# Performance work log

Hardware: AMD Instinct MI355X
Metric: run time of the kernel (lower is better)

The kernel has to match this reference:

```python
import jax, jax.numpy as jnp
import numpy as np

STATE = 1024

def setup_inputs() -> dict:
    key = jax.random.key(0)
    k1, k2, k3, k4, k5 = jax.random.split(key, 5)
    B, IN, S = 4096, 1024, STATE
    stdv = 1.0 / np.sqrt(S)
    return {
        "input": jax.random.normal(k1, (B, IN), jnp.float32),
        "old_h": jax.random.normal(k2, (B, S), jnp.float32),
        "old_cell": jax.random.normal(k3, (B, S), jnp.float32),
        "weights": jax.random.uniform(k4, (4 * S, IN + S), jnp.float32, -stdv, stdv),
        "bias": jax.random.uniform(k5, (4 * S,), jnp.float32, -stdv, stdv),
    }

def reference(input, old_h, old_cell, weights, bias):
    # Fused gate GEMM: X = [input, old_h] -> [B, IN+S]; gates -> [B, 4S]
    X = jnp.concatenate([input, old_h], axis=1)
    gates = X @ weights.T + bias
    f, i, o, g = jnp.split(gates, 4, axis=1)
    f = jax.nn.sigmoid(f)
    i = jax.nn.sigmoid(i)
    o = jax.nn.sigmoid(o)
    g = jnp.tanh(g)
    new_cell = f * old_cell + i * g
    new_h = o * jnp.tanh(new_cell)
    return new_h, new_cell
```

## Files before the change

### kernel.cpp

```cpp
#include <hip/hip_runtime.h>
#include <stdint.h>

#define NB   4096
#define KD   2048
#define ND   4096
#define SD   1024

#define BM   256
#define BN   256
#define BK   64
#define NKT  (KD / BK)

using f32x4  = __attribute__((ext_vector_type(4))) float;
using bf16x8 = __attribute__((ext_vector_type(8))) short;

typedef const __attribute__((address_space(1))) uint32_t* gas_u32;
typedef __attribute__((address_space(3))) uint32_t* las_u32;

__device__ __forceinline__ unsigned short f2bf(float f) {
    union { float f; uint32_t u; } c; c.f = f;
    uint32_t u = c.u;
    uint32_t r = (u + 0x7fffu + ((u >> 16) & 1u)) >> 16;
    return (unsigned short)r;
}

__device__ __forceinline__ void async_load16(const void* gsrc, void* ldst) {
    __builtin_amdgcn_global_load_lds((gas_u32)gsrc, (las_u32)ldst, 16, 0, 0);
}

__device__ __forceinline__ float frcp(float x) { return __builtin_amdgcn_rcpf(x); }
__device__ __forceinline__ float sigm(float x) { return frcp(1.f + __expf(-x)); }
__device__ __forceinline__ float tanh_fast(float x) {
    return 1.f - 2.f * frcp(1.f + __expf(2.f * x));
}

__global__ void pack_kernel(const float* __restrict__ input,
                            const float* __restrict__ old_h,
                            const float* __restrict__ weights,
                            const float* __restrict__ bias,
                            unsigned short* __restrict__ Xb,
                            unsigned short* __restrict__ Wb,
                            float* __restrict__ biasR) {
    const int XCH = NB * (KD / 4);
    const int WCH = ND * (KD / 4);
    const int BCH = ND / 4;
    const int total = XCH + WCH + BCH;
    for (int c = blockIdx.x * blockDim.x + threadIdx.x; c < total;
         c += gridDim.x * blockDim.x) {
        if (c < XCH) {
            int b  = c >> 9;
            int k  = (c & 511) << 2;
            const float* src = (k < 1024) ? (input + (size_t)b * 1024 + k)
                                          : (old_h + (size_t)b * 1024 + (k - 1024));
            float4 v = *reinterpret_cast<const float4*>(src);
            ushort4 o;
            o.x = f2bf(v.x); o.y = f2bf(v.y); o.z = f2bf(v.z); o.w = f2bf(v.w);
            *reinterpret_cast<ushort4*>(Xb + (size_t)b * KD + k) = o;
        } else if (c < XCH + WCH) {
            int cc = c - XCH;
            int n  = cc >> 9;
            int k  = (cc & 511) << 2;
            int srow = ((n >> 4) & 3) * SD + ((n >> 6) * 16 + (n & 15));
            float4 v = *reinterpret_cast<const float4*>(weights + (size_t)srow * KD + k);
            ushort4 o;
            o.x = f2bf(v.x); o.y = f2bf(v.y); o.z = f2bf(v.z); o.w = f2bf(v.w);
            *reinterpret_cast<ushort4*>(Wb + (size_t)n * KD + k) = o;
        } else {
            int n4 = (c - XCH - WCH) << 2;
            #pragma unroll
            for (int t = 0; t < 4; ++t) {
                int n = n4 + t;
                biasR[n] = bias[((n >> 4) & 3) * SD + ((n >> 6) * 16 + (n & 15))];
            }
        }
    }
}

#define SEG(DB, AB, HALF) (((((DB) * 2 + (AB)) * 2) + (HALF)) * 8192)

#define SBAR   __builtin_amdgcn_s_barrier()
#define SFENCE __builtin_amdgcn_sched_barrier(0)
#define ASM_LGKM0  asm volatile("s_waitcnt lgkmcnt(0)" ::: "memory")
#define ASM_VMCNT2 asm volatile("s_waitcnt vmcnt(2)" ::: "memory")
#define ASM_VMCNT8 asm volatile("s_waitcnt vmcnt(8)" ::: "memory")

__launch_bounds__(512, 2)
__global__ void lstm_gemm(const unsigned short* __restrict__ Xb,
                          const unsigned short* __restrict__ Wb,
                          const float* __restrict__ biasR,
                          const float* __restrict__ old_cell,
                          float* __restrict__ new_h,
                          float* __restrict__ new_cell) {
    __shared__ unsigned short lds[65536];

    const int tid  = threadIdx.x;
    const int lane = tid & 63;
    const int wid  = tid >> 6;
    const int wm   = wid >> 2;
    const int wn   = wid & 3;
    const int l15  = lane & 15;
    const int krow = lane >> 4;

    const int wg    = blockIdx.x;
    const int swz   = (wg & 7) * 32 + (wg >> 3);
    const int mblk  = swz >> 4;
    const int nblk  = swz & 15;
    const int rbase = mblk * BM;
    const int nbase = nblk * BN;

    const int c0 = tid, c1 = tid + 512;
    const int srow0 = c0 >> 3, sk0 = ((c0 & 7) ^ (srow0 & 7)) * 8;
    const int srow1 = c1 >> 3, sk1 = ((c1 & 7) ^ (srow1 & 7)) * 8;

    f32x4  acc[8][4] = {};
    bf16x8 a[4][2];
    bf16x8 bm[2][2];
    bf16x8 ba[2][2];

#define STAGE(PTR, TB, KT, DB, AB, HALF) do {                                   \
        async_load16((PTR) + (size_t)((TB) + (HALF) * 128 + srow0) * KD +       \
                         (KT) * BK + sk0,                                       \
                     lds + SEG(DB, AB, HALF) + c0 * 8);                         \
        async_load16((PTR) + (size_t)((TB) + (HALF) * 128 + srow1) * KD +       \
                         (KT) * BK + sk1,                                       \
                     lds + SEG(DB, AB, HALF) + c1 * 8);                         \
    } while (0)

#define LOAD_A(DB, MQ) do {                                                     \
        const unsigned short* base_ = lds + SEG(DB, 0, 0) + wm * 8192;          \
        _Pragma("unroll") for (int i_ = 0; i_ < 4; ++i_)                        \
        _Pragma("unroll") for (int kk_ = 0; kk_ < 2; ++kk_) {                   \
            int r_ = (MQ) * 64 + i_ * 16 + l15;                                 \
            int s_ = kk_ * 4 + krow;                                            \
            a[i_][kk_] = *reinterpret_cast<const bf16x8*>(                      \
                base_ + r_ * 64 + ((s_ ^ (r_ & 7)) * 8));                       \
        }                                                                       \
    } while (0)

#define LOAD_B_TO(DST, DB, NQ) do {                                             \
        const unsigned short* base_ = lds + SEG(DB, 1, 0) + (wn >> 1) * 8192;   \
        _Pragma("unroll") for (int j_ = 0; j_ < 2; ++j_)                        \
        _Pragma("unroll") for (int kk_ = 0; kk_ < 2; ++kk_) {                   \
            int r_ = (wn & 1) * 64 + ((NQ) * 2 + j_) * 16 + l15;                \
            int s_ = kk_ * 4 + krow;                                            \
            DST[j_][kk_] = *reinterpret_cast<const bf16x8*>(                    \
                base_ + r_ * 64 + ((s_ ^ (r_ & 7)) * 8));                       \
        }                                                                       \
    } while (0)

#define MMA_Q(MQ, NQH, BB) do {                                                 \
        _Pragma("unroll") for (int i_ = 0; i_ < 4; ++i_)                        \
        _Pragma("unroll") for (int j_ = 0; j_ < 2; ++j_)                        \
        _Pragma("unroll") for (int kk_ = 0; kk_ < 2; ++kk_)                     \
            acc[(MQ) * 4 + i_][(NQH) * 2 + j_] =                                \
                __builtin_amdgcn_mfma_f32_16x16x32_bf16(                        \
                    a[i_][kk_], BB[j_][kk_],                                    \
                    acc[(MQ) * 4 + i_][(NQH) * 2 + j_], 0, 0, 0);               \
    } while (0)

#define PH_HEAD   SFENCE; ASM_LGKM0; SBAR; SFENCE; __builtin_amdgcn_s_setprio(1)
#define PH_HEADV  SFENCE; ASM_LGKM0; ASM_VMCNT2; SBAR; SFENCE; __builtin_amdgcn_s_setprio(1)
#define PRIO0     __builtin_amdgcn_s_setprio(0)

    STAGE(Wb, nbase, 0, 0, 1, 0);
    STAGE(Wb, nbase, 0, 0, 1, 1);
    STAGE(Xb, rbase, 0, 0, 0, 0);
    STAGE(Xb, rbase, 0, 0, 0, 1);
    STAGE(Wb, nbase, 1, 1, 1, 0);
    STAGE(Wb, nbase, 1, 1, 1, 1);
    STAGE(Xb, rbase, 1, 1, 0, 0);
    STAGE(Xb, rbase, 1, 1, 0, 1);
    ASM_VMCNT8;
    SBAR; SFENCE;
    LOAD_B_TO(bm, 0, 0);
    LOAD_A(0, 0);

#define KBODY(TT, BUF) do {                                                     \
        const int kt2_ = ((TT) + 2) & (NKT - 1);                                \
                                                                        \
        PH_HEAD;  MMA_Q(0, 0, bm); LOAD_B_TO(ba, BUF, 1);       PRIO0;          \
                                                                        \
        PH_HEAD;  MMA_Q(0, 1, ba); LOAD_A(BUF, 1);              PRIO0;          \
        STAGE(Wb, nbase, kt2_, BUF, 1, 0);                                      \
                                                                        \
        PH_HEADV; MMA_Q(1, 0, bm); LOAD_B_TO(bm, (BUF) ^ 1, 0); PRIO0;          \
        STAGE(Wb, nbase, kt2_, BUF, 1, 1);                                      \
        STAGE(Xb, rbase, kt2_, BUF, 0, 0);                                      \
                                                                        \
        PH_HEAD;  MMA_Q(1, 1, ba); LOAD_A((BUF) ^ 1, 0);        PRIO0;          \
        STAGE(Xb, rbase, kt2_, BUF, 0, 1);                                      \
    } while (0)

    for (int t = 0; t < NKT; t += 2) {
        KBODY(t, 0);
        KBODY(t + 1, 1);
    }

    const int s = (nblk * 4 + wn) * 16 + l15;
    float bg[4];
    #pragma unroll
    for (int jj = 0; jj < 4; ++jj)
        bg[jj] = biasR[nbase + wn * 64 + jj * 16 + l15];

    #pragma unroll
    for (int mi = 0; mi < 8; ++mi) {
        #pragma unroll
        for (int r = 0; r < 4; ++r) {
            const int row = rbase + wm * 128 + mi * 16 + krow * 4 + r;
            float fg = sigm(acc[mi][0][r] + bg[0]);
            float ig = sigm(acc[mi][1][r] + bg[1]);
            float og = sigm(acc[mi][2][r] + bg[2]);
            float gg = tanh_fast(acc[mi][3][r] + bg[3]);
            float oc = old_cell[(size_t)row * SD + s];
            float nc = fmaf(fg, oc, ig * gg);
            float nh = og * tanh_fast(nc);
            new_h[(size_t)row * SD + s]    = nh;
            new_cell[(size_t)row * SD + s] = nc;
        }
    }
}

extern "C" void kernel_launch(void* const* d_in, const int* in_sizes, int n_in,
                              void* d_out, int out_size, void* d_ws, size_t ws_size,
                              hipStream_t stream) {
    const float* input    = (const float*)d_in[0];
    const float* old_h    = (const float*)d_in[1];
    const float* old_cell = (const float*)d_in[2];
    const float* weights  = (const float*)d_in[3];
    const float* bias     = (const float*)d_in[4];

    unsigned short* Xb  = (unsigned short*)d_ws;
    unsigned short* Wb  = (unsigned short*)((char*)d_ws + (size_t)16777216);
    float*          bR  = (float*)((char*)d_ws + (size_t)33554432);

    float* out_h = (float*)d_out;
    float* out_c = out_h + (size_t)NB * SD;

    pack_kernel<<<2048, 256, 0, stream>>>(input, old_h, weights, bias, Xb, Wb, bR);
    lstm_gemm<<<(NB / BM) * (ND / BN), 512, 0, stream>>>(Xb, Wb, bR, old_cell,
                                                         out_h, out_c);
}
```

Measured before the change: 77.27 us.

## Interleave MFMA with LDS reads and global stages via sched_group_barrier

```diff
diff --git a/kernel.cpp b/kernel.cpp
--- a/kernel.cpp
+++ b/kernel.cpp
@@ -80,8 +80,9 @@
 
 #define SBAR   __builtin_amdgcn_s_barrier()
 #define SFENCE __builtin_amdgcn_sched_barrier(0)
+#define SGB(M, N)  __builtin_amdgcn_sched_group_barrier((M), (N), 0)
 #define ASM_LGKM0  asm volatile("s_waitcnt lgkmcnt(0)" ::: "memory")
-#define ASM_VMCNT2 asm volatile("s_waitcnt vmcnt(2)" ::: "memory")
+#define ASM_VMCNT4 asm volatile("s_waitcnt vmcnt(4)" ::: "memory")
 #define ASM_VMCNT8 asm volatile("s_waitcnt vmcnt(8)" ::: "memory")
 
 __launch_bounds__(512, 2)
@@ -158,9 +159,26 @@
                     acc[(MQ) * 4 + i_][(NQH) * 2 + j_], 0, 0, 0);               \
     } while (0)
 
+#define MMA_Q_JK(MQ, NQH, BB) do {                                              \
+        _Pragma("unroll") for (int j_ = 0; j_ < 2; ++j_)                        \
+        _Pragma("unroll") for (int kk_ = 0; kk_ < 2; ++kk_)                     \
+        _Pragma("unroll") for (int i_ = 0; i_ < 4; ++i_)                        \
+            acc[(MQ) * 4 + i_][(NQH) * 2 + j_] =                                \
+                __builtin_amdgcn_mfma_f32_16x16x32_bf16(                        \
+                    a[i_][kk_], BB[j_][kk_],                                    \
+                    acc[(MQ) * 4 + i_][(NQH) * 2 + j_], 0, 0, 0);               \
+    } while (0)
+
 #define PH_HEAD   SFENCE; ASM_LGKM0; SBAR; SFENCE; __builtin_amdgcn_s_setprio(1)
-#define PH_HEADV  SFENCE; ASM_LGKM0; ASM_VMCNT2; SBAR; SFENCE; __builtin_amdgcn_s_setprio(1)
+#define PH_HEADV  SFENCE; ASM_LGKM0; ASM_VMCNT4; SBAR; SFENCE; __builtin_amdgcn_s_setprio(1)
 #define PRIO0     __builtin_amdgcn_s_setprio(0)
+
+#define SGB_Q0  _Pragma("unroll") for (int g_ = 0; g_ < 4; ++g_) { SGB(0x100, 1); SGB(0x8, 4); }
+#define SGB_Q1  SGB(0x70, 4);                                                   \
+                _Pragma("unroll") for (int g_ = 0; g_ < 4; ++g_) { SGB(0x8, 4); SGB(0x100, 2); }
+#define SGB_Q2  SGB(0x70, 4);                                                   \
+                _Pragma("unroll") for (int g_ = 0; g_ < 4; ++g_) { SGB(0x8, 4); SGB(0x100, 1); }
+#define SGB_Q3  _Pragma("unroll") for (int g_ = 0; g_ < 4; ++g_) { SGB(0x8, 4); SGB(0x100, 2); }
 
     STAGE(Wb, nbase, 0, 0, 1, 0);
     STAGE(Wb, nbase, 0, 0, 1, 1);
@@ -177,18 +195,34 @@
 
 #define KBODY(TT, BUF) do {                                                     \
         const int kt2_ = ((TT) + 2) & (NKT - 1);                                \
-                                                                        \
-        PH_HEAD;  MMA_Q(0, 0, bm); LOAD_B_TO(ba, BUF, 1);       PRIO0;          \
-                                                                        \
-        PH_HEAD;  MMA_Q(0, 1, ba); LOAD_A(BUF, 1);              PRIO0;          \
+               \
+        PH_HEAD;                                                                \
+        MMA_Q(0, 0, bm);                                                        \
+        LOAD_B_TO(ba, BUF, 1);                                                  \
+        SGB_Q0;                                                                 \
+        PRIO0;                                                                  \
+                           \
+        PH_HEAD;                                                                \
         STAGE(Wb, nbase, kt2_, BUF, 1, 0);                                      \
-                                                                        \
-        PH_HEADV; MMA_Q(1, 0, bm); LOAD_B_TO(bm, (BUF) ^ 1, 0); PRIO0;          \
         STAGE(Wb, nbase, kt2_, BUF, 1, 1);                                      \
+        MMA_Q(0, 1, ba);                                                        \
+        LOAD_A(BUF, 1);                                                         \
+        SGB_Q1;                                                                 \
+        PRIO0;                                                                  \
+          \
+        PH_HEADV;                                                               \
         STAGE(Xb, rbase, kt2_, BUF, 0, 0);                                      \
-                                                                        \
-        PH_HEAD;  MMA_Q(1, 1, ba); LOAD_A((BUF) ^ 1, 0);        PRIO0;          \
         STAGE(Xb, rbase, kt2_, BUF, 0, 1);                                      \
+        MMA_Q_JK(1, 0, bm);                                                     \
+        LOAD_B_TO(bm, (BUF) ^ 1, 0);                                            \
+        SGB_Q2;                                                                 \
+        PRIO0;                                                                  \
+                                       \
+        PH_HEAD;                                                                \
+        MMA_Q(1, 1, ba);                                                        \
+        LOAD_A((BUF) ^ 1, 0);                                                   \
+        SGB_Q3;                                                                 \
+        PRIO0;                                                                  \
     } while (0)
 
     for (int t = 0; t < NKT; t += 2) {
```

Result: slower. 79.94 us (+3.5%).

## Restructure K-loop into two k-half phases with sched_group_barrier interleaving

Applied to the files above, without the earlier changes.

```diff
diff --git a/kernel.cpp b/kernel.cpp
--- a/kernel.cpp
+++ b/kernel.cpp
@@ -80,8 +80,9 @@
 
 #define SBAR   __builtin_amdgcn_s_barrier()
 #define SFENCE __builtin_amdgcn_sched_barrier(0)
+#define SGB(M, N)  __builtin_amdgcn_sched_group_barrier((M), (N), 0)
 #define ASM_LGKM0  asm volatile("s_waitcnt lgkmcnt(0)" ::: "memory")
-#define ASM_VMCNT2 asm volatile("s_waitcnt vmcnt(2)" ::: "memory")
+#define ASM_VMCNT0 asm volatile("s_waitcnt vmcnt(0)" ::: "memory")
 #define ASM_VMCNT8 asm volatile("s_waitcnt vmcnt(8)" ::: "memory")
 
 __launch_bounds__(512, 2)
@@ -113,9 +114,8 @@
     const int srow1 = c1 >> 3, sk1 = ((c1 & 7) ^ (srow1 & 7)) * 8;
 
     f32x4  acc[8][4] = {};
-    bf16x8 a[4][2];
-    bf16x8 bm[2][2];
-    bf16x8 ba[2][2];
+    bf16x8 aA[8], aB[8];
+    bf16x8 bA[4], bB[4];
 
 #define STAGE(PTR, TB, KT, DB, AB, HALF) do {                                   \
         async_load16((PTR) + (size_t)((TB) + (HALF) * 128 + srow0) * KD +       \
@@ -126,41 +126,32 @@
                      lds + SEG(DB, AB, HALF) + c1 * 8);                         \
     } while (0)
 
-#define LOAD_A(DB, MQ) do {                                                     \
+#define LOAD_AH(SET, DB, KK) do {                                               \
         const unsigned short* base_ = lds + SEG(DB, 0, 0) + wm * 8192;          \
-        _Pragma("unroll") for (int i_ = 0; i_ < 4; ++i_)                        \
-        _Pragma("unroll") for (int kk_ = 0; kk_ < 2; ++kk_) {                   \
-            int r_ = (MQ) * 64 + i_ * 16 + l15;                                 \
-            int s_ = kk_ * 4 + krow;                                            \
-            a[i_][kk_] = *reinterpret_cast<const bf16x8*>(                      \
+        _Pragma("unroll") for (int i_ = 0; i_ < 8; ++i_) {                      \
+            int r_ = i_ * 16 + l15;                                             \
+            int s_ = (KK) * 4 + krow;                                           \
+            SET[i_] = *reinterpret_cast<const bf16x8*>(                         \
                 base_ + r_ * 64 + ((s_ ^ (r_ & 7)) * 8));                       \
         }                                                                       \
     } while (0)
 
-#define LOAD_B_TO(DST, DB, NQ) do {                                             \
+#define LOAD_BH(SET, DB, KK) do {                                               \
         const unsigned short* base_ = lds + SEG(DB, 1, 0) + (wn >> 1) * 8192;   \
-        _Pragma("unroll") for (int j_ = 0; j_ < 2; ++j_)                        \
-        _Pragma("unroll") for (int kk_ = 0; kk_ < 2; ++kk_) {                   \
-            int r_ = (wn & 1) * 64 + ((NQ) * 2 + j_) * 16 + l15;                \
-            int s_ = kk_ * 4 + krow;                                            \
-            DST[j_][kk_] = *reinterpret_cast<const bf16x8*>(                    \
+        _Pragma("unroll") for (int j_ = 0; j_ < 4; ++j_) {                      \
+            int r_ = (wn & 1) * 64 + j_ * 16 + l15;                             \
+            int s_ = (KK) * 4 + krow;                                           \
+            SET[j_] = *reinterpret_cast<const bf16x8*>(                         \
                 base_ + r_ * 64 + ((s_ ^ (r_ & 7)) * 8));                       \
         }                                                                       \
     } while (0)
 
-#define MMA_Q(MQ, NQH, BB) do {                                                 \
-        _Pragma("unroll") for (int i_ = 0; i_ < 4; ++i_)                        \
-        _Pragma("unroll") for (int j_ = 0; j_ < 2; ++j_)                        \
-        _Pragma("unroll") for (int kk_ = 0; kk_ < 2; ++kk_)                     \
-            acc[(MQ) * 4 + i_][(NQH) * 2 + j_] =                                \
-                __builtin_amdgcn_mfma_f32_16x16x32_bf16(                        \
-                    a[i_][kk_], BB[j_][kk_],                                    \
-                    acc[(MQ) * 4 + i_][(NQH) * 2 + j_], 0, 0, 0);               \
-    } while (0)
-
-#define PH_HEAD   SFENCE; ASM_LGKM0; SBAR; SFENCE; __builtin_amdgcn_s_setprio(1)
-#define PH_HEADV  SFENCE; ASM_LGKM0; ASM_VMCNT2; SBAR; SFENCE; __builtin_amdgcn_s_setprio(1)
-#define PRIO0     __builtin_amdgcn_s_setprio(0)
+#define MMA32(ASET, BSET) do {                                                  \
+        _Pragma("unroll") for (int i_ = 0; i_ < 8; ++i_)                        \
+        _Pragma("unroll") for (int j_ = 0; j_ < 4; ++j_)                        \
+            acc[i_][j_] = __builtin_amdgcn_mfma_f32_16x16x32_bf16(              \
+                ASET[i_], BSET[j_], acc[i_][j_], 0, 0, 0);                      \
+    } while (0)
 
     STAGE(Wb, nbase, 0, 0, 1, 0);
     STAGE(Wb, nbase, 0, 0, 1, 1);
@@ -172,23 +163,27 @@
     STAGE(Xb, rbase, 1, 1, 0, 1);
     ASM_VMCNT8;
     SBAR; SFENCE;
-    LOAD_B_TO(bm, 0, 0);
-    LOAD_A(0, 0);
+    LOAD_AH(aA, 0, 0);
+    LOAD_BH(bA, 0, 0);
 
 #define KBODY(TT, BUF) do {                                                     \
         const int kt2_ = ((TT) + 2) & (NKT - 1);                                \
-                                                                        \
-        PH_HEAD;  MMA_Q(0, 0, bm); LOAD_B_TO(ba, BUF, 1);       PRIO0;          \
-                                                                        \
-        PH_HEAD;  MMA_Q(0, 1, ba); LOAD_A(BUF, 1);              PRIO0;          \
+                             \
+        LOAD_AH(aB, BUF, 1);                                                    \
+        LOAD_BH(bB, BUF, 1);                                                    \
+        MMA32(aA, bA);                                                          \
+        SGB(0x100, 12); SGB(0x8, 32);                                           \
+        ASM_LGKM0; ASM_VMCNT0; SBAR; SFENCE;                                    \
+          \
+        STAGE(Xb, rbase, kt2_, BUF, 0, 0);                                      \
+        STAGE(Xb, rbase, kt2_, BUF, 0, 1);                                      \
         STAGE(Wb, nbase, kt2_, BUF, 1, 0);                                      \
-                                                                        \
-        PH_HEADV; MMA_Q(1, 0, bm); LOAD_B_TO(bm, (BUF) ^ 1, 0); PRIO0;          \
         STAGE(Wb, nbase, kt2_, BUF, 1, 1);                                      \
-        STAGE(Xb, rbase, kt2_, BUF, 0, 0);                                      \
-                                                                        \
-        PH_HEAD;  MMA_Q(1, 1, ba); LOAD_A((BUF) ^ 1, 0);        PRIO0;          \
-        STAGE(Xb, rbase, kt2_, BUF, 0, 1);                                      \
+        LOAD_AH(aA, (BUF) ^ 1, 0);                                              \
+        LOAD_BH(bA, (BUF) ^ 1, 0);                                              \
+        MMA32(aB, bB);                                                          \
+        SGB(0x30, 8); SGB(0x100, 12); SGB(0x8, 32);                             \
+        SBAR; SFENCE;                                                           \
     } while (0)
 
     for (int t = 0; t < NKT; t += 2) {
```

After: 80.19 us. 1.04x slower.
